# Kernel tuning notes

Hardware: AMD Instinct MI355X
Metric: run time of the kernel (lower is better)

Reference implementation:

```python
import jax, jax.numpy as jnp
import numpy as np


def setup_inputs() -> dict:
    key = jax.random.key(0)
    k1, k2, k3, k4 = jax.random.split(key, 4)
    B, C, L = 16, 512, 4096
    x = jax.random.normal(k1, (B, C, L), dtype=jnp.float32)
    # conv1d kernel_size=1, bias=False -> weight [3C, C]
    w_qkv = jax.random.normal(k2, (3 * C, C), dtype=jnp.float32) * (1.0 / np.sqrt(C))
    w_out = jax.random.normal(k3, (C, C), dtype=jnp.float32) * (1.0 / np.sqrt(C))
    b_out = jax.random.normal(k4, (C,), dtype=jnp.float32) * 0.01
    return {"x": x, "w_qkv": w_qkv, "w_out": w_out, "b_out": b_out}


def reference(x, w_qkv, w_out, b_out):
    # x: [b, c, l]; 1x1 conv == channel-wise matmul
    qkv = jnp.einsum('bcl,oc->bol', x, w_qkv)          # [b, 3c, l]
    q, k, v = jnp.split(qkv, 3, axis=1)                 # each [b, c, l] (heads=1)
    k = jax.nn.softmax(k, axis=-1)                      # softmax over sequence dim l
    context = jnp.einsum('bdn,ben->bde', k, v)          # [b, c, c]
    out = jnp.einsum('bde,bdn->ben', context, q)        # [b, c, l]
    return jnp.einsum('bcl,oc->bol', out, w_out) + b_out[None, :, None]
```

## Files before the change

### kernel.cpp

```cpp
#include <hip/hip_runtime.h>
#include <hip/hip_bf16.h>
#include <type_traits>

#define DEVINL __device__ __forceinline__

typedef float f32x4 __attribute__((ext_vector_type(4)));
typedef __bf16 bf16x8 __attribute__((ext_vector_type(8)));

DEVINL float bf2f(short s) {
  unsigned u = ((unsigned)(unsigned short)s) << 16;
  float f; __builtin_memcpy(&f, &u, 4); return f;
}
DEVINL short f2bf(float f) {
  unsigned u; __builtin_memcpy(&u, &f, 4);
  u += 0x7fff + ((u >> 16) & 1);
  return (short)(u >> 16);
}

DEVINL void gl_lds16(const void* g, void* l) {
  __builtin_amdgcn_global_load_lds(
      (const __attribute__((address_space(1))) void*)g,
      (__attribute__((address_space(3))) void*)l, 16, 0, 0);
}

template <typename OutT, bool BIAS>
DEVINL void epilogue_store(f32x4 (&acc)[4][4], char* smem,
                           OutT* __restrict__ C, int ldc, int m0, int n0,
                           const float* __restrict__ bias, int t) {
  const int wave = t >> 6, lane = t & 63;
  const int quad = lane >> 4, l16 = lane & 15;
  const int arow = (wave >> 1) * 64, brow = (wave & 1) * 64;
  if constexpr (std::is_same<OutT, float>::value) {
    float* tile = (float*)smem;
#pragma unroll
    for (int rnd = 0; rnd < 2; ++rnd) {
      if ((arow >> 6) == rnd) {
#pragma unroll
        for (int mi = 0; mi < 4; ++mi)
#pragma unroll
          for (int ni = 0; ni < 4; ++ni) {
            const int col = brow + ni * 16 + l16;
#pragma unroll
            for (int r = 0; r < 4; ++r) {
              const int row = mi * 16 + quad * 4 + r;
              float v = acc[mi][ni][r];
              if (BIAS) v += bias[m0 + rnd * 64 + row];
              tile[row * 128 + col] = v;
            }
          }
      }
      __syncthreads();
#pragma unroll
      for (int i = 0; i < 8; ++i) {
        const int row = wave * 16 + i * 2 + (lane >> 5);
        const int cf  = (lane & 31) * 4;
        f32x4 v = *(f32x4*)&tile[row * 128 + cf];
        *(f32x4*)&C[(long)(m0 + rnd * 64 + row) * ldc + n0 + cf] = v;
      }
      __syncthreads();
    }
  } else {
    short* tile = (short*)smem;
#pragma unroll
    for (int mi = 0; mi < 4; ++mi)
#pragma unroll
      for (int ni = 0; ni < 4; ++ni) {
        const int col = brow + ni * 16 + l16;
#pragma unroll
        for (int r = 0; r < 4; ++r) {
          const int row = arow + mi * 16 + quad * 4 + r;
          float v = acc[mi][ni][r];
          if (BIAS) v += bias[m0 + row];
          tile[row * 128 + col] = f2bf(v);
        }
      }
    __syncthreads();
#pragma unroll
    for (int i = 0; i < 8; ++i) {
      const int row = wave * 32 + i * 4 + (lane >> 4);
      const int cs  = l16 * 8;
      int4 v = *(int4*)&tile[row * 128 + cs];
      *(int4*)&C[(long)(m0 + row) * ldc + n0 + cs] = v;
    }
  }
}

template <typename OutT, bool BIAS>
__global__ __launch_bounds__(256, 4)
void gemm_nt(const short* __restrict__ A, long sA, int lda,
             const short* __restrict__ B, long sB, int ldb,
             OutT* __restrict__ C, long sC, int ldc,
             const float* __restrict__ bias, int K)
{
  A += (long)blockIdx.z * sA;
  B += (long)blockIdx.z * sB;
  C += (long)blockIdx.z * sC;

  __shared__ char smem[32768];
  short* As = (short*)smem;
  short* Bs = (short*)(smem + 8192);

  const int t    = threadIdx.x;
  const int wave = t >> 6, lane = t & 63;
  const int quad = lane >> 4, l16 = lane & 15;
  const int m0 = blockIdx.y * 128, n0 = blockIdx.x * 128;
  const int lrow = t >> 2;
  const int lk8  = (t & 3) * 8;
  const int arow = (wave >> 1) * 64, brow = (wave & 1) * 64;

  f32x4 acc[4][4];
#pragma unroll
  for (int i = 0; i < 4; ++i)
#pragma unroll
    for (int j = 0; j < 4; ++j) acc[i][j] = (f32x4){0.f, 0.f, 0.f, 0.f};

  for (int k0 = 0; k0 < K; k0 += 32) {
#pragma unroll
    for (int s = 0; s < 2; ++s) {
      gl_lds16(A + (long)(m0 + s * 64 + lrow) * lda + k0 + lk8,
               (char*)As + s * 4096 + wave * 1024);
      gl_lds16(B + (long)(n0 + s * 64 + lrow) * ldb + k0 + lk8,
               (char*)Bs + s * 4096 + wave * 1024);
    }
    __syncthreads();

    bf16x8 af[4], bfr[4];
#pragma unroll
    for (int i = 0; i < 4; ++i)
      af[i] = *(const bf16x8*)&As[(arow + i * 16 + l16) * 32 + quad * 8];
#pragma unroll
    for (int i = 0; i < 4; ++i)
      bfr[i] = *(const bf16x8*)&Bs[(brow + i * 16 + l16) * 32 + quad * 8];

#pragma unroll
    for (int mi = 0; mi < 4; ++mi)
#pragma unroll
      for (int ni = 0; ni < 4; ++ni)
        acc[mi][ni] = __builtin_amdgcn_mfma_f32_16x16x32_bf16(
            af[mi], bfr[ni], acc[mi][ni], 0, 0, 0);
    __syncthreads();
  }

  epilogue_store<OutT, BIAS>(acc, smem, C, ldc, m0, n0, bias, t);
}

__global__ __launch_bounds__(256, 4)
void gemm_sk(const short* __restrict__ Ab, const short* __restrict__ Bb,
             float* __restrict__ Cp)
{
  const int b = blockIdx.z >> 2, s = blockIdx.z & 3;
  const short* A = Ab + (long)b * 2097152;
  const short* B = Bb + (long)b * 2097152;
  float* C = Cp + (long)(s * 16 + b) * 262144;

  __shared__ char smem[32768];
  short* As = (short*)smem;
  short* Bs = (short*)(smem + 8192);

  const int t    = threadIdx.x;
  const int wave = t >> 6, lane = t & 63;
  const int quad = lane >> 4, l16 = lane & 15;
  const int m0 = blockIdx.y * 128, n0 = blockIdx.x * 128;
  const int lrow = t >> 2;
  const int lk8  = (t & 3) * 8;
  const int arow = (wave >> 1) * 64, brow = (wave & 1) * 64;
  const int kbeg = s * 1024, kend = kbeg + 1024;

  f32x4 acc[4][4];
#pragma unroll
  for (int i = 0; i < 4; ++i)
#pragma unroll
    for (int j = 0; j < 4; ++j) acc[i][j] = (f32x4){0.f, 0.f, 0.f, 0.f};

  for (int k0 = kbeg; k0 < kend; k0 += 32) {
#pragma unroll
    for (int sb = 0; sb < 2; ++sb) {
      gl_lds16(A + (long)(m0 + sb * 64 + lrow) * 4096 + k0 + lk8,
               (char*)As + sb * 4096 + wave * 1024);
      gl_lds16(B + (long)(n0 + sb * 64 + lrow) * 4096 + k0 + lk8,
               (char*)Bs + sb * 4096 + wave * 1024);
    }
    __syncthreads();

    bf16x8 af[4], bfr[4];
#pragma unroll
    for (int i = 0; i < 4; ++i)
      af[i] = *(const bf16x8*)&As[(arow + i * 16 + l16) * 32 + quad * 8];
#pragma unroll
    for (int i = 0; i < 4; ++i)
      bfr[i] = *(const bf16x8*)&Bs[(brow + i * 16 + l16) * 32 + quad * 8];

#pragma unroll
    for (int mi = 0; mi < 4; ++mi)
#pragma unroll
      for (int ni = 0; ni < 4; ++ni)
        acc[mi][ni] = __builtin_amdgcn_mfma_f32_16x16x32_bf16(
            af[mi], bfr[ni], acc[mi][ni], 0, 0, 0);
    __syncthreads();
  }

  epilogue_store<float, false>(acc, smem, C, 512, m0, n0, nullptr, t);
}

__global__ void reduce_sk(const float* __restrict__ p, short* __restrict__ o) {
  const long i = ((long)blockIdx.x * 256 + threadIdx.x) * 4;
  f32x4 a = *(const f32x4*)&p[i];
  f32x4 b = *(const f32x4*)&p[i + 4194304];
  f32x4 c = *(const f32x4*)&p[i + 2 * 4194304];
  f32x4 d = *(const f32x4*)&p[i + 3 * 4194304];
  short r[4];
#pragma unroll
  for (int j = 0; j < 4; ++j) r[j] = f2bf(a[j] + b[j] + c[j] + d[j]);
  *(long*)&o[i] = *(long*)r;
}

__global__ void transpose_cast(const float* __restrict__ x,
                               short* __restrict__ xT, short* __restrict__ xb)
{
  __shared__ float tile[32][33];
  x  += (long)blockIdx.z * 2097152;
  xT += (long)blockIdx.z * 2097152;
  xb += (long)blockIdx.z * 2097152;
  const int l0 = blockIdx.x * 32, c0 = blockIdx.y * 32;
  const int tx = threadIdx.x, ty = threadIdx.y;
#pragma unroll
  for (int i = 0; i < 4; ++i) {
    float v = x[(long)(c0 + ty + i * 8) * 4096 + l0 + tx];
    tile[ty + i * 8][tx] = v;
    xb[(long)(c0 + ty + i * 8) * 4096 + l0 + tx] = f2bf(v);
  }
  __syncthreads();
#pragma unroll
  for (int i = 0; i < 4; ++i)
    xT[(long)(l0 + ty + i * 8) * 512 + c0 + tx] = f2bf(tile[tx][ty + i * 8]);
}

DEVINL float to_f(float v) { return v; }
DEVINL float to_f(short v) { return bf2f(v); }

template <typename InT, typename OutT>
__global__ void transpose_k(const InT* __restrict__ src, OutT* __restrict__ dst,
                            int R, int Cc, long ss, long ds)
{
  __shared__ float tile[32][33];
  src += (long)blockIdx.z * ss;
  dst += (long)blockIdx.z * ds;
  const int c0 = blockIdx.x * 32, r0 = blockIdx.y * 32;
  const int tx = threadIdx.x, ty = threadIdx.y;
#pragma unroll
  for (int i = 0; i < 4; ++i)
    tile[ty + i * 8][tx] = to_f(src[(long)(r0 + ty + i * 8) * Cc + c0 + tx]);
  __syncthreads();
#pragma unroll
  for (int i = 0; i < 4; ++i) {
    float v = tile[tx][ty + i * 8];
    if constexpr (std::is_same<OutT, float>::value)
      dst[(long)(c0 + ty + i * 8) * R + r0 + tx] = v;
    else
      dst[(long)(c0 + ty + i * 8) * R + r0 + tx] = f2bf(v);
  }
}

__global__ void cast_weights(const float* __restrict__ wq, short* __restrict__ wqb,
                             const float* __restrict__ wo, short* __restrict__ wob) {
  const int i = blockIdx.x * 256 + threadIdx.x;
  if (i < 786432) wqb[i] = f2bf(wq[i]);
  else            wob[i - 786432] = f2bf(wo[i - 786432]);
}

__global__ void softmax_rows(short* __restrict__ k) {
  const int b = blockIdx.x >> 9, d = blockIdx.x & 511;
  short* p = k + (long)b * 2097152 + (long)d * 4096;
  const int t = threadIdx.x, wave = t >> 6, lane = t & 63;

  short v16[16];
  *(int4*)&v16[0] = *(const int4*)&p[t * 8];
  *(int4*)&v16[8] = *(const int4*)&p[2048 + t * 8];

  float vals[16];
  float m = -1e30f;
#pragma unroll
  for (int i = 0; i < 16; ++i) {
    vals[i] = bf2f(v16[i]);
    m = fmaxf(m, vals[i]);
  }
  for (int off = 32; off; off >>= 1) m = fmaxf(m, __shfl_xor(m, off));
  __shared__ float redm[4], reds[4];
  if (lane == 0) redm[wave] = m;
  __syncthreads();
  m = fmaxf(fmaxf(redm[0], redm[1]), fmaxf(redm[2], redm[3]));

  float s = 0.f;
#pragma unroll
  for (int i = 0; i < 16; ++i) { vals[i] = __expf(vals[i] - m); s += vals[i]; }
  for (int off = 32; off; off >>= 1) s += __shfl_xor(s, off);
  if (lane == 0) reds[wave] = s;
  __syncthreads();
  s = reds[0] + reds[1] + reds[2] + reds[3];
  const float inv = 1.f / s;
#pragma unroll
  for (int i = 0; i < 16; ++i) v16[i] = f2bf(vals[i] * inv);
  *(int4*)&p[t * 8] = *(int4*)&v16[0];
  *(int4*)&p[2048 + t * 8] = *(int4*)&v16[8];
}

extern "C" void kernel_launch(void* const* d_in, const int* in_sizes, int n_in,
                              void* d_out, int out_size, void* d_ws, size_t ws_size,
                              hipStream_t stream) {
  const float* x     = (const float*)d_in[0];
  const float* w_qkv = (const float*)d_in[1];
  const float* w_out = (const float*)d_in[2];
  const float* b_out = (const float*)d_in[3];
  float* out = (float*)d_out;

  const long CL = (long)512 * 4096;
  const long CC = (long)512 * 512;

  char* ws = (char*)d_ws;
  short* xT  = (short*)(ws);
  short* xb  = (short*)(ws + 67108864);
  short* kbf = (short*)(ws + 134217728);
  float* Pp  = (float*)(ws + 201326592);
  short* P   = (short*)(ws + 268435456);
  short* ctx = (short*)(ws + 276824064);
  short* M2  = (short*)(ws + 285212672);
  short* M3  = (short*)(ws + 293601280);
  short* wqb = (short*)(ws + 301989888);
  short* wob = (short*)(ws + 303562752);
  short* wqT = (short*)(ws + 304087040);

  cast_weights<<<4096, 256, 0, stream>>>(w_qkv, wqb, w_out, wob);

  transpose_k<float, short><<<dim3(16, 16, 1), dim3(32, 8), 0, stream>>>(
      w_qkv, wqT, 512, 512, 0, 0);

  transpose_cast<<<dim3(128, 16, 16), dim3(32, 8), 0, stream>>>(x, xT, xb);

  gemm_nt<short, false><<<dim3(32, 4, 16), 256, 0, stream>>>(
      wqb + 512 * 512, 0, 512, xT, CL, 512, kbf, CL, 4096, nullptr, 512);

  softmax_rows<<<16 * 512, 256, 0, stream>>>(kbf);

  gemm_sk<<<dim3(4, 4, 64), 256, 0, stream>>>(kbf, xb, Pp);
  reduce_sk<<<4096, 256, 0, stream>>>(Pp, P);

  gemm_nt<short, false><<<dim3(4, 4, 16), 256, 0, stream>>>(
      P, CC, 512, wqb + 2 * 512 * 512, 0, 512, ctx, CC, 512, nullptr, 512);

  gemm_nt<short, false><<<dim3(4, 4, 16), 256, 0, stream>>>(
      wob, 0, 512, ctx, CC, 512, M2, CC, 512, nullptr, 512);

  gemm_nt<short, false><<<dim3(4, 4, 16), 256, 0, stream>>>(
      M2, CC, 512, wqT, 0, 512, M3, CC, 512, nullptr, 512);

  gemm_nt<float, true><<<dim3(32, 4, 16), 256, 0, stream>>>(
      M3, CC, 512, xT, CL, 512, out, CL, 4096, b_out, 512);
}
```

Baseline: 536.8 us.

## Fuse key softmax exp into K-projection GEMM epilogue and defer normalization

Drops the separate softmax kernel. The K-projection GEMM epilogue now applies exp and accumulates per-row sums with atomics, and the 1/sum normalization moves into the split-K reduction of the context product. This removes a full read and write pass over the 128 MB bf16 key tensor. It also adds an XCD-aware block swizzle to the GEMMs. In exchange, softmax runs without max subtraction, so large logits could overflow, and the row-sum accumulation is nondeterministic because of the atomics.

```diff
diff --git a/kernel.cpp b/kernel.cpp
--- a/kernel.cpp
+++ b/kernel.cpp
@@ -23,10 +23,23 @@
       (__attribute__((address_space(3))) void*)l, 16, 0, 0);
 }
 
-template <typename OutT, bool BIAS>
+DEVINL void swz_blk(int& bx, int& by, int& bz) {
+  const int gx = gridDim.x, gy = gridDim.y;
+  const int tpz = gx * gy;
+  const int nwg = tpz * gridDim.z;
+  int fid = bx + gx * (by + gy * bz);
+  fid = (fid & 7) * (nwg >> 3) + (fid >> 3);
+  bz = fid / tpz;
+  const int r = fid - bz * tpz;
+  by = r % gy;
+  bx = r / gy;
+}
+
+template <typename OutT, bool BIAS, bool EXP>
 DEVINL void epilogue_store(f32x4 (&acc)[4][4], char* smem,
                            OutT* __restrict__ C, int ldc, int m0, int n0,
-                           const float* __restrict__ bias, int t) {
+                           const float* __restrict__ bias,
+                           float* __restrict__ rowsum, int t) {
   const int wave = t >> 6, lane = t & 63;
   const int quad = lane >> 4, l16 = lane & 15;
   const int arow = (wave >> 1) * 64, brow = (wave & 1) * 64;
@@ -64,14 +77,21 @@
 #pragma unroll
     for (int mi = 0; mi < 4; ++mi)
 #pragma unroll
-      for (int ni = 0; ni < 4; ++ni) {
-        const int col = brow + ni * 16 + l16;
-#pragma unroll
-        for (int r = 0; r < 4; ++r) {
-          const int row = arow + mi * 16 + quad * 4 + r;
+      for (int r = 0; r < 4; ++r) {
+        const int row = arow + mi * 16 + quad * 4 + r;
+        float rs = 0.f;
+#pragma unroll
+        for (int ni = 0; ni < 4; ++ni) {
+          const int col = brow + ni * 16 + l16;
           float v = acc[mi][ni][r];
           if (BIAS) v += bias[m0 + row];
+          if (EXP) { v = __expf(v); rs += v; }
           tile[row * 128 + col] = f2bf(v);
+        }
+        if (EXP) {
+          rs += __shfl_xor(rs, 1); rs += __shfl_xor(rs, 2);
+          rs += __shfl_xor(rs, 4); rs += __shfl_xor(rs, 8);
+          if (l16 == 0) atomicAdd(&rowsum[m0 + row], rs);
         }
       }
     __syncthreads();
@@ -85,16 +105,20 @@
   }
 }
 
-template <typename OutT, bool BIAS>
+template <typename OutT, bool BIAS, bool EXP>
 __global__ __launch_bounds__(256, 4)
 void gemm_nt(const short* __restrict__ A, long sA, int lda,
              const short* __restrict__ B, long sB, int ldb,
              OutT* __restrict__ C, long sC, int ldc,
-             const float* __restrict__ bias, int K)
+             const float* __restrict__ bias, float* __restrict__ rowsum, int K)
 {
-  A += (long)blockIdx.z * sA;
-  B += (long)blockIdx.z * sB;
-  C += (long)blockIdx.z * sC;
+  int bx = blockIdx.x, by = blockIdx.y, bz = blockIdx.z;
+  swz_blk(bx, by, bz);
+
+  A += (long)bz * sA;
+  B += (long)bz * sB;
+  C += (long)bz * sC;
+  if (EXP) rowsum += (long)bz * 512;
 
   __shared__ char smem[32768];
   short* As = (short*)smem;
@@ -103,7 +127,7 @@
   const int t    = threadIdx.x;
   const int wave = t >> 6, lane = t & 63;
   const int quad = lane >> 4, l16 = lane & 15;
-  const int m0 = blockIdx.y * 128, n0 = blockIdx.x * 128;
+  const int m0 = by * 128, n0 = bx * 128;
   const int lrow = t >> 2;
   const int lk8  = (t & 3) * 8;
   const int arow = (wave >> 1) * 64, brow = (wave & 1) * 64;
@@ -141,14 +165,17 @@
     __syncthreads();
   }
 
-  epilogue_store<OutT, BIAS>(acc, smem, C, ldc, m0, n0, bias, t);
+  epilogue_store<OutT, BIAS, EXP>(acc, smem, C, ldc, m0, n0, bias, rowsum, t);
 }
 
 __global__ __launch_bounds__(256, 4)
 void gemm_sk(const short* __restrict__ Ab, const short* __restrict__ Bb,
              float* __restrict__ Cp)
 {
-  const int b = blockIdx.z >> 2, s = blockIdx.z & 3;
+  int bx = blockIdx.x, by = blockIdx.y, bz = blockIdx.z;
+  swz_blk(bx, by, bz);
+
+  const int b = bz >> 2, s = bz & 3;
   const short* A = Ab + (long)b * 2097152;
   const short* B = Bb + (long)b * 2097152;
   float* C = Cp + (long)(s * 16 + b) * 262144;
@@ -160,7 +187,7 @@
   const int t    = threadIdx.x;
   const int wave = t >> 6, lane = t & 63;
   const int quad = lane >> 4, l16 = lane & 15;
-  const int m0 = blockIdx.y * 128, n0 = blockIdx.x * 128;
+  const int m0 = by * 128, n0 = bx * 128;
   const int lrow = t >> 2;
   const int lk8  = (t & 3) * 8;
   const int arow = (wave >> 1) * 64, brow = (wave & 1) * 64;
@@ -199,18 +226,21 @@
     __syncthreads();
   }
 
-  epilogue_store<float, false>(acc, smem, C, 512, m0, n0, nullptr, t);
-}
-
-__global__ void reduce_sk(const float* __restrict__ p, short* __restrict__ o) {
+  epilogue_store<float, false, false>(acc, smem, C, 512, m0, n0, nullptr,
+                                      nullptr, t);
+}
+
+__global__ void reduce_sk(const float* __restrict__ p, short* __restrict__ o,
+                          const float* __restrict__ s) {
   const long i = ((long)blockIdx.x * 256 + threadIdx.x) * 4;
+  const float inv = 1.f / s[i >> 9];
   f32x4 a = *(const f32x4*)&p[i];
   f32x4 b = *(const f32x4*)&p[i + 4194304];
   f32x4 c = *(const f32x4*)&p[i + 2 * 4194304];
   f32x4 d = *(const f32x4*)&p[i + 3 * 4194304];
   short r[4];
 #pragma unroll
-  for (int j = 0; j < 4; ++j) r[j] = f2bf(a[j] + b[j] + c[j] + d[j]);
+  for (int j = 0; j < 4; ++j) r[j] = f2bf((a[j] + b[j] + c[j] + d[j]) * inv);
   *(long*)&o[i] = *(long*)r;
 }
 
@@ -262,46 +292,12 @@
 }
 
 __global__ void cast_weights(const float* __restrict__ wq, short* __restrict__ wqb,
-                             const float* __restrict__ wo, short* __restrict__ wob) {
+                             const float* __restrict__ wo, short* __restrict__ wob,
+                             float* __restrict__ ssum) {
   const int i = blockIdx.x * 256 + threadIdx.x;
+  if (blockIdx.x < 32) ssum[i] = 0.f;
   if (i < 786432) wqb[i] = f2bf(wq[i]);
   else            wob[i - 786432] = f2bf(wo[i - 786432]);
-}
-
-__global__ void softmax_rows(short* __restrict__ k) {
-  const int b = blockIdx.x >> 9, d = blockIdx.x & 511;
-  short* p = k + (long)b * 2097152 + (long)d * 4096;
-  const int t = threadIdx.x, wave = t >> 6, lane = t & 63;
-
-  short v16[16];
-  *(int4*)&v16[0] = *(const int4*)&p[t * 8];
-  *(int4*)&v16[8] = *(const int4*)&p[2048 + t * 8];
-
-  float vals[16];
-  float m = -1e30f;
-#pragma unroll
-  for (int i = 0; i < 16; ++i) {
-    vals[i] = bf2f(v16[i]);
-    m = fmaxf(m, vals[i]);
-  }
-  for (int off = 32; off; off >>= 1) m = fmaxf(m, __shfl_xor(m, off));
-  __shared__ float redm[4], reds[4];
-  if (lane == 0) redm[wave] = m;
-  __syncthreads();
-  m = fmaxf(fmaxf(redm[0], redm[1]), fmaxf(redm[2], redm[3]));
-
-  float s = 0.f;
-#pragma unroll
-  for (int i = 0; i < 16; ++i) { vals[i] = __expf(vals[i] - m); s += vals[i]; }
-  for (int off = 32; off; off >>= 1) s += __shfl_xor(s, off);
-  if (lane == 0) reds[wave] = s;
-  __syncthreads();
-  s = reds[0] + reds[1] + reds[2] + reds[3];
-  const float inv = 1.f / s;
-#pragma unroll
-  for (int i = 0; i < 16; ++i) v16[i] = f2bf(vals[i] * inv);
-  *(int4*)&p[t * 8] = *(int4*)&v16[0];
-  *(int4*)&p[2048 + t * 8] = *(int4*)&v16[8];
 }
 
 extern "C" void kernel_launch(void* const* d_in, const int* in_sizes, int n_in,
@@ -328,31 +324,30 @@
   short* wqb = (short*)(ws + 301989888);
   short* wob = (short*)(ws + 303562752);
   short* wqT = (short*)(ws + 304087040);
-
-  cast_weights<<<4096, 256, 0, stream>>>(w_qkv, wqb, w_out, wob);
+  float* ssum = (float*)(ws + 293601280);
+
+  cast_weights<<<4096, 256, 0, stream>>>(w_qkv, wqb, w_out, wob, ssum);
 
   transpose_k<float, short><<<dim3(16, 16, 1), dim3(32, 8), 0, stream>>>(
       w_qkv, wqT, 512, 512, 0, 0);
 
   transpose_cast<<<dim3(128, 16, 16), dim3(32, 8), 0, stream>>>(x, xT, xb);
 
-  gemm_nt<short, false><<<dim3(32, 4, 16), 256, 0, stream>>>(
-      wqb + 512 * 512, 0, 512, xT, CL, 512, kbf, CL, 4096, nullptr, 512);
-
-  softmax_rows<<<16 * 512, 256, 0, stream>>>(kbf);
+  gemm_nt<short, false, true><<<dim3(32, 4, 16), 256, 0, stream>>>(
+      wqb + 512 * 512, 0, 512, xT, CL, 512, kbf, CL, 4096, nullptr, ssum, 512);
 
   gemm_sk<<<dim3(4, 4, 64), 256, 0, stream>>>(kbf, xb, Pp);
-  reduce_sk<<<4096, 256, 0, stream>>>(Pp, P);
-
-  gemm_nt<short, false><<<dim3(4, 4, 16), 256, 0, stream>>>(
-      P, CC, 512, wqb + 2 * 512 * 512, 0, 512, ctx, CC, 512, nullptr, 512);
-
-  gemm_nt<short, false><<<dim3(4, 4, 16), 256, 0, stream>>>(
-      wob, 0, 512, ctx, CC, 512, M2, CC, 512, nullptr, 512);
-
-  gemm_nt<short, false><<<dim3(4, 4, 16), 256, 0, stream>>>(
-      M2, CC, 512, wqT, 0, 512, M3, CC, 512, nullptr, 512);
-
-  gemm_nt<float, true><<<dim3(32, 4, 16), 256, 0, stream>>>(
-      M3, CC, 512, xT, CL, 512, out, CL, 4096, b_out, 512);
-}
+  reduce_sk<<<4096, 256, 0, stream>>>(Pp, P, ssum);
+
+  gemm_nt<short, false, false><<<dim3(4, 4, 16), 256, 0, stream>>>(
+      P, CC, 512, wqb + 2 * 512 * 512, 0, 512, ctx, CC, 512, nullptr, nullptr, 512);
+
+  gemm_nt<short, false, false><<<dim3(4, 4, 16), 256, 0, stream>>>(
+      wob, 0, 512, ctx, CC, 512, M2, CC, 512, nullptr, nullptr, 512);
+
+  gemm_nt<short, false, false><<<dim3(4, 4, 16), 256, 0, stream>>>(
+      M2, CC, 512, wqT, 0, 512, M3, CC, 512, nullptr, nullptr, 512);
+
+  gemm_nt<float, true, false><<<dim3(32, 4, 16), 256, 0, stream>>>(
+      M3, CC, 512, xT, CL, 512, out, CL, 4096, b_out, nullptr, 512);
+}
```

Result: faster. 511.9 us (-4.6%).
